# Kernel optimization log

Hardware: AMD Instinct MI355X
Metric: run time of the kernel (lower is better)

Reference implementation:

```python
import jax, jax.numpy as jnp
import numpy as np

N_NODES = 50000   # nodes per channel
N_EDGES = 800000  # intra edges per channel (avg degree ~16)
N_GRAPHS = 64     # graphs in the batch (global_add_pool segments)
D = 128           # node_features_len == out_channels
L = 3             # n_layers
BN_EPS = 1e-5
NEG_SLOPE = 0.01  # F.leaky_relu default


def setup_inputs() -> dict:
    key = jax.random.key(0)
    ks = jax.random.split(key, 24)
    s = 0.05
    inp = {
        "x1": jax.random.normal(ks[0], (N_NODES, D), jnp.float32),
        "x2": jax.random.normal(ks[1], (N_NODES, D), jnp.float32),
        # GIN MLP channel 1: Linear-BN-ReLU-Linear-ReLU, stacked over layers
        "W1_ch1": jax.random.normal(ks[2], (L, D, D), jnp.float32) * s,
        "b1_ch1": jax.random.normal(ks[3], (L, D), jnp.float32) * s,
        "bn_g": 1.0 + jax.random.normal(ks[4], (L, D), jnp.float32) * s,
        "bn_b": jax.random.normal(ks[5], (L, D), jnp.float32) * s,
        "bn_m": jax.random.normal(ks[6], (L, D), jnp.float32) * s,
        "bn_v": 0.5 + jax.random.uniform(ks[7], (L, D), jnp.float32),
        "W2_ch1": jax.random.normal(ks[8], (L, D, D), jnp.float32) * s,
        "b2_ch1": jax.random.normal(ks[9], (L, D), jnp.float32) * s,
        # GIN MLP channel 2: Linear-ReLU-Linear
        "W1_ch2": jax.random.normal(ks[10], (L, D, D), jnp.float32) * s,
        "b1_ch2": jax.random.normal(ks[11], (L, D), jnp.float32) * s,
        "W2_ch2": jax.random.normal(ks[12], (L, D, D), jnp.float32) * s,
        "b2_ch2": jax.random.normal(ks[13], (L, D), jnp.float32) * s,
        # head: Linear(2*D*L -> D) - ReLU - Dropout - Linear(D -> 1)
        "Wf1": jax.random.normal(ks[14], (2 * D * L, D), jnp.float32) * s,
        "bf1": jax.random.normal(ks[15], (D,), jnp.float32) * s,
        "Wf2": jax.random.normal(ks[16], (D, 1), jnp.float32) * s,
        "bf2": jax.random.normal(ks[17], (1,), jnp.float32) * s,
        "edge1": jax.random.randint(ks[18], (2, N_EDGES), 0, N_NODES, dtype=jnp.int32),
        "edge2": jax.random.randint(ks[19], (2, N_EDGES), 0, N_NODES, dtype=jnp.int32),
        "batch1": jnp.sort(jax.random.randint(ks[20], (N_NODES,), 0, N_GRAPHS, dtype=jnp.int32)),
        "batch2": jnp.sort(jax.random.randint(ks[21], (N_NODES,), 0, N_GRAPHS, dtype=jnp.int32)),
    }
    return inp


def _aggregate(x, edge):
    # GINConv sum aggregation: message x[src] scattered to dst; eps=0 default
    return jax.ops.segment_sum(x[edge[0]], edge[1], num_segments=N_NODES)


def _channel1(x, edge, batch, W1, b1, g, b, m, v, W2, b2):
    pooled = []
    for i in range(L):
        h = (x + _aggregate(x, edge)) @ W1[i] + b1[i]
        h = (h - m[i]) * (g[i] / jnp.sqrt(v[i] + BN_EPS)) + b[i]  # eval-mode BN
        h = jax.nn.relu(h)
        h = jax.nn.relu(h @ W2[i] + b2[i])
        x = jax.nn.leaky_relu(h, NEG_SLOPE)
        pooled.append(jax.ops.segment_sum(x, batch, num_segments=N_GRAPHS))
    return jnp.concatenate(pooled, axis=-1)  # [G, D*L]


def _channel2(x, edge, batch, W1, b1, W2, b2):
    pooled = []
    for i in range(L):
        h = jax.nn.relu((x + _aggregate(x, edge)) @ W1[i] + b1[i])
        h = h @ W2[i] + b2[i]
        x = jax.nn.leaky_relu(h, NEG_SLOPE)
        pooled.append(jax.ops.segment_sum(x, batch, num_segments=N_GRAPHS))
    return jnp.concatenate(pooled, axis=-1)  # [G, D*L]


def reference(x1, x2, W1_ch1, b1_ch1, bn_g, bn_b, bn_m, bn_v, W2_ch1, b2_ch1,
              W1_ch2, b1_ch2, W2_ch2, b2_ch2, Wf1, bf1, Wf2, bf2,
              edge1, edge2, batch1, batch2):
    p1 = _channel1(x1, edge1, batch1, W1_ch1, b1_ch1, bn_g, bn_b, bn_m, bn_v, W2_ch1, b2_ch1)
    p2 = _channel2(x2, edge2, batch2, W1_ch2, b1_ch2, W2_ch2, b2_ch2)
    z = jnp.concatenate([p1, p2], axis=-1)  # [G, 2*D*L]
    h = jax.nn.relu(z @ Wf1 + bf1)          # dropout is identity in eval mode
    return h @ Wf2 + bf2                    # [G, 1]
```

## Files before the change

### kernel.cpp

```cpp
#include <hip/hip_runtime.h>

#define NN 50000
#define NE 800000
#define NG 64
#define DD 128
#define NL 3
#define ZW (2 * DD * NL)
#define NB2 128
#define NPB 391
#define CAP2 8192
#define CHUNK 4096
#define P1B 196
#define GB2 1024

typedef __attribute__((ext_vector_type(8))) short short8;
typedef __attribute__((ext_vector_type(4))) float f32x4;

__device__ inline unsigned short f2bf(float f) {
  unsigned int u = __float_as_uint(f);
  unsigned int r = (u + 0x7fffu + ((u >> 16) & 1u)) >> 16;
  return (unsigned short)r;
}

__global__ __launch_bounds__(256) void cvt_bf16_kernel(const float* __restrict__ in,
                                                       unsigned short* __restrict__ out, int n8) {
  int i = blockIdx.x * 256 + threadIdx.x;
  if (i >= n8) return;
  const float4* in4 = reinterpret_cast<const float4*>(in);
  float4 a = in4[2 * i], b = in4[2 * i + 1];
  uint4 o;
  o.x = (unsigned int)f2bf(a.x) | ((unsigned int)f2bf(a.y) << 16);
  o.y = (unsigned int)f2bf(a.z) | ((unsigned int)f2bf(a.w) << 16);
  o.z = (unsigned int)f2bf(b.x) | ((unsigned int)f2bf(b.y) << 16);
  o.w = (unsigned int)f2bf(b.z) | ((unsigned int)f2bf(b.w) << 16);
  reinterpret_cast<uint4*>(out)[i] = o;
}

__global__ __launch_bounds__(256) void cvt_wt_kernel(const float* __restrict__ in,
                                                     unsigned short* __restrict__ out) {
  __shared__ float tile[32][33];
  int mat = blockIdx.z;
  int k0 = blockIdx.x * 32, c0 = blockIdx.y * 32;
  int tx = threadIdx.x & 31, ty = threadIdx.x >> 5;
  const float* ip = in + mat * 16384;
  unsigned short* op = out + mat * 16384;
#pragma unroll
  for (int rr = 0; rr < 32; rr += 8)
    tile[ty + rr][tx] = ip[(k0 + ty + rr) * 128 + (c0 + tx)];
  __syncthreads();
#pragma unroll
  for (int rr = 0; rr < 32; rr += 8)
    op[(c0 + ty + rr) * 128 + (k0 + tx)] = f2bf(tile[tx][ty + rr]);
}

__global__ __launch_bounds__(256) void bucket_kernel(const int* __restrict__ e1,
                                                     const int* __restrict__ e2,
                                                     int* __restrict__ bcur,
                                                     uint2* __restrict__ pairs) {
  int ch = blockIdx.x >= P1B;
  int blk = blockIdx.x - ch * P1B;
  const int* E = ch ? e2 : e1;
  int base = blk * CHUNK;
  __shared__ int lcnt[NB2], gbase[NB2];
  for (int i = threadIdx.x; i < NB2; i += 256) lcnt[i] = 0;
  __syncthreads();
  int srcv[16], dstv[16], lrank[16];
#pragma unroll
  for (int k = 0; k < 16; k++) {
    int e = base + k * 256 + threadIdx.x;
    if (e < NE) {
      srcv[k] = E[e];
      dstv[k] = E[NE + e];
      lrank[k] = atomicAdd(&lcnt[dstv[k] / NPB], 1);
    } else dstv[k] = -1;
  }
  __syncthreads();
  for (int i = threadIdx.x; i < NB2; i += 256)
    gbase[i] = atomicAdd(&bcur[ch * NB2 + i], lcnt[i]);
  __syncthreads();
#pragma unroll
  for (int k = 0; k < 16; k++)
    if (dstv[k] >= 0) {
      int g = dstv[k] / NPB;
      pairs[(size_t)(ch * NB2 + g) * CAP2 + gbase[g] + lrank[k]] =
          make_uint2((unsigned)srcv[k], (unsigned)dstv[k]);
    }
}

__global__ __launch_bounds__(256) void scan_bcur_kernel(const int* __restrict__ bcur,
                                                        int* __restrict__ colbase) {
  __shared__ int s[256];
  int tid = threadIdx.x;
  int v = bcur[tid];
  s[tid] = v;
  __syncthreads();
  int segstart = tid & ~127;
  for (int o = 1; o < 128; o <<= 1) {
    int t = (tid - o >= segstart) ? s[tid - o] : 0;
    __syncthreads();
    s[tid] += t;
    __syncthreads();
  }
  colbase[tid] = s[tid] - v;
}

__global__ __launch_bounds__(256) void csr_build_kernel(const uint2* __restrict__ pairs,
                                                        const int* __restrict__ bcur,
                                                        const int* __restrict__ colbase,
                                                        int* __restrict__ rowptr,
                                                        int* __restrict__ col) {
  int g = blockIdx.x;
  int ch = g >> 7, b = g & 127;
  int node0 = b * NPB;
  int nloc = min(NPB, NN - node0);
  int count = bcur[g];
  int base = colbase[g];
  const uint2* p = pairs + (size_t)g * CAP2;
  __shared__ int hist[512], pref[512], cur[512], stmp[256];
  for (int i = threadIdx.x; i < 512; i += 256) hist[i] = 0;
  __syncthreads();
  for (int e = threadIdx.x; e < count; e += 256)
    atomicAdd(&hist[(int)p[e].y - node0], 1);
  __syncthreads();
  int t = threadIdx.x;
  int a0 = hist[2 * t], a1 = hist[2 * t + 1];
  int sum = a0 + a1;
  stmp[t] = sum;
  __syncthreads();
  for (int o = 1; o < 256; o <<= 1) {
    int tv = (t >= o) ? stmp[t - o] : 0;
    __syncthreads();
    stmp[t] += tv;
    __syncthreads();
  }
  int ex = stmp[t] - sum;
  pref[2 * t] = ex;       pref[2 * t + 1] = ex + a0;
  cur[2 * t] = ex;        cur[2 * t + 1] = ex + a0;
  __syncthreads();
  for (int i = threadIdx.x; i < nloc; i += 256)
    rowptr[ch * (NN + 1) + node0 + i] = base + pref[i];
  if (threadIdx.x == 0 && b == NB2 - 1) rowptr[ch * (NN + 1) + NN] = base + count;
  for (int e = threadIdx.x; e < count; e += 256) {
    uint2 pr = p[e];
    int pos = atomicAdd(&cur[(int)pr.y - node0], 1);
    col[ch * NE + base + pos] = (int)pr.x;
  }
}

__global__ __launch_bounds__(256) void gstart_kernel(const int* __restrict__ batch1,
                                                     const int* __restrict__ batch2,
                                                     int* __restrict__ gstart) {
  int t = threadIdx.x;
  if (t >= 2 * (NG + 1)) return;
  int ch = t / (NG + 1), g = t % (NG + 1);
  const int* b = ch ? batch2 : batch1;
  int lo = 0, hi = NN;
  while (lo < hi) {
    int m = (lo + hi) >> 1;
    if (b[m] < g) lo = m + 1; else hi = m;
  }
  gstart[t] = lo;
}

__global__ __launch_bounds__(256) void agg_kernel(const unsigned short* __restrict__ X,
                                                  const int* __restrict__ rowptr,
                                                  const int* __restrict__ col,
                                                  unsigned short* __restrict__ Y) {
  int node = blockIdx.x * 16 + (threadIdx.x >> 4);
  int lane = threadIdx.x & 15;
  int ch = node >= NN;
  int nl = node - ch * NN;
  const int* rp = rowptr + ch * (NN + 1);
  const int* cl = col + ch * NE;
  const uint4* X4 = reinterpret_cast<const uint4*>(X);
  size_t chbase = (size_t)ch * NN * 16;
  float acc[8];
  {
    uint4 sv = X4[(size_t)node * 16 + lane];
    unsigned int w[4] = {sv.x, sv.y, sv.z, sv.w};
#pragma unroll
    for (int q = 0; q < 4; q++) {
      acc[2 * q]     = __uint_as_float(w[q] << 16);
      acc[2 * q + 1] = __uint_as_float(w[q] & 0xffff0000u);
    }
  }
  int s = rp[nl], e = rp[nl + 1];
  int j = s;
  for (; j + 8 <= e; j += 8) {
    uint4 v[8];
#pragma unroll
    for (int q = 0; q < 8; q++)
      v[q] = X4[chbase + (size_t)cl[j + q] * 16 + lane];
#pragma unroll
    for (int q = 0; q < 8; q++) {
      unsigned int w[4] = {v[q].x, v[q].y, v[q].z, v[q].w};
#pragma unroll
      for (int t = 0; t < 4; t++) {
        acc[2 * t]     += __uint_as_float(w[t] << 16);
        acc[2 * t + 1] += __uint_as_float(w[t] & 0xffff0000u);
      }
    }
  }
  for (; j < e; ++j) {
    uint4 v = X4[chbase + (size_t)cl[j] * 16 + lane];
    unsigned int w[4] = {v.x, v.y, v.z, v.w};
#pragma unroll
    for (int t = 0; t < 4; t++) {
      acc[2 * t]     += __uint_as_float(w[t] << 16);
      acc[2 * t + 1] += __uint_as_float(w[t] & 0xffff0000u);
    }
  }
  uint4 o;
  unsigned int* ow = reinterpret_cast<unsigned int*>(&o);
#pragma unroll
  for (int q = 0; q < 4; q++)
    ow[q] = (unsigned int)f2bf(acc[2 * q]) | ((unsigned int)f2bf(acc[2 * q + 1]) << 16);
  reinterpret_cast<uint4*>(Y)[(size_t)node * 16 + lane] = o;
}

__global__ __launch_bounds__(256) void gemm_fused_kernel(
    const unsigned short* __restrict__ Y, unsigned short* __restrict__ X,
    const unsigned short* __restrict__ WT,
    const float* __restrict__ b1c1, const float* __restrict__ b1c2,
    const float* __restrict__ b2c1, const float* __restrict__ b2c2,
    const float* __restrict__ bng, const float* __restrict__ bnb,
    const float* __restrict__ bnm, const float* __restrict__ bnv, int layer) {
  __shared__ unsigned short hlds[16][136];
  int ch = blockIdx.x >= GB2;
  int lane = threadIdx.x & 63, wv = threadIdx.x >> 6;
  int l15 = lane & 15, lk = lane >> 4;
  int c0 = wv * 32;
  const unsigned short* W1 = WT + (size_t)(ch * 6 + layer) * 16384;
  const unsigned short* W2 = WT + (size_t)(ch * 6 + 3 + layer) * 16384;
  short8 w1f[2][4], w2f[2][4];
#pragma unroll
  for (int ct = 0; ct < 2; ct++)
#pragma unroll
    for (int kk = 0; kk < 4; kk++) {
      size_t boff = (size_t)(c0 + ct * 16 + l15) * 128 + kk * 32 + lk * 8;
      w1f[ct][kk] = *reinterpret_cast<const short8*>(W1 + boff);
      w2f[ct][kk] = *reinterpret_cast<const short8*>(W2 + boff);
    }
  const float* b1 = (ch ? b1c2 : b1c1) + layer * DD;
  const float* b2 = (ch ? b2c2 : b2c1) + layer * DD;
  float sc1[2], sh1[2], sh2[2];
#pragma unroll
  for (int ct = 0; ct < 2; ct++) {
    int colg = c0 + ct * 16 + l15;
    if (!ch) {
      float s = bng[layer * DD + colg] * rsqrtf(bnv[layer * DD + colg] + 1e-5f);
      sc1[ct] = s;
      sh1[ct] = (b1[colg] - bnm[layer * DD + colg]) * s + bnb[layer * DD + colg];
    } else {
      sc1[ct] = 1.f;
      sh1[ct] = b1[colg];
    }
    sh2[ct] = b2[colg];
  }
  for (int t = (ch ? blockIdx.x - GB2 : blockIdx.x); t < 3125; t += GB2) {
    int r0l = t * 16;
    size_t r0g = (size_t)ch * NN + r0l;
    const unsigned short* yp = Y + (r0g + l15) * 128 + lk * 8;
    short8 a0 = *reinterpret_cast<const short8*>(yp);
    short8 a1 = *reinterpret_cast<const short8*>(yp + 32);
    short8 a2 = *reinterpret_cast<const short8*>(yp + 64);
    short8 a3 = *reinterpret_cast<const short8*>(yp + 96);
#pragma unroll
    for (int ct = 0; ct < 2; ct++) {
      f32x4 acc = {0.f, 0.f, 0.f, 0.f};
      acc = __builtin_amdgcn_mfma_f32_16x16x32_bf16(a0, w1f[ct][0], acc, 0, 0, 0);
      acc = __builtin_amdgcn_mfma_f32_16x16x32_bf16(a1, w1f[ct][1], acc, 0, 0, 0);
      acc = __builtin_amdgcn_mfma_f32_16x16x32_bf16(a2, w1f[ct][2], acc, 0, 0, 0);
      acc = __builtin_amdgcn_mfma_f32_16x16x32_bf16(a3, w1f[ct][3], acc, 0, 0, 0);
      int colg = c0 + ct * 16 + l15;
#pragma unroll
      for (int r = 0; r < 4; r++) {
        float tv = fmaxf(acc[r] * sc1[ct] + sh1[ct], 0.f);
        hlds[lk * 4 + r][colg] = f2bf(tv);
      }
    }
    __syncthreads();
    short8 h0 = *reinterpret_cast<const short8*>(&hlds[l15][lk * 8]);
    short8 h1 = *reinterpret_cast<const short8*>(&hlds[l15][32 + lk * 8]);
    short8 h2 = *reinterpret_cast<const short8*>(&hlds[l15][64 + lk * 8]);
    short8 h3 = *reinterpret_cast<const short8*>(&hlds[l15][96 + lk * 8]);
#pragma unroll
    for (int ct = 0; ct < 2; ct++) {
      f32x4 acc = {0.f, 0.f, 0.f, 0.f};
      acc = __builtin_amdgcn_mfma_f32_16x16x32_bf16(h0, w2f[ct][0], acc, 0, 0, 0);
      acc = __builtin_amdgcn_mfma_f32_16x16x32_bf16(h1, w2f[ct][1], acc, 0, 0, 0);
      acc = __builtin_amdgcn_mfma_f32_16x16x32_bf16(h2, w2f[ct][2], acc, 0, 0, 0);
      acc = __builtin_amdgcn_mfma_f32_16x16x32_bf16(h3, w2f[ct][3], acc, 0, 0, 0);
      int colg = c0 + ct * 16 + l15;
#pragma unroll
      for (int r = 0; r < 4; r++) {
        float tv = acc[r] + sh2[ct];
        if (!ch) tv = fmaxf(tv, 0.f);
        else     tv = tv > 0.f ? tv : 0.01f * tv;
        X[(r0g + lk * 4 + r) * 128 + colg] = f2bf(tv);
      }
    }
    __syncthreads();
  }
}

__global__ __launch_bounds__(256) void pool_kernel(const unsigned short* __restrict__ X,
                                                   const int* __restrict__ gstart,
                                                   float* __restrict__ z, int layer) {
  int ch = blockIdx.x >> 6, g = blockIdx.x & 63;
  int r0 = gstart[ch * (NG + 1) + g], r1 = gstart[ch * (NG + 1) + g + 1];
  int c8 = threadIdx.x & 15, part = threadIdx.x >> 4;
  const uint4* X4 = reinterpret_cast<const uint4*>(X);
  size_t base = (size_t)ch * NN * 16 + c8;
  float acc[8];
#pragma unroll
  for (int q = 0; q < 8; q++) acc[q] = 0.f;
  int r = r0 + part;
  for (; r + 48 < r1; r += 64) {
    uint4 v0 = X4[base + (size_t)r * 16];
    uint4 v1 = X4[base + (size_t)(r + 16) * 16];
    uint4 v2 = X4[base + (size_t)(r + 32) * 16];
    uint4 v3 = X4[base + (size_t)(r + 48) * 16];
    unsigned int w0[4] = {v0.x, v0.y, v0.z, v0.w};
    unsigned int w1[4] = {v1.x, v1.y, v1.z, v1.w};
    unsigned int w2[4] = {v2.x, v2.y, v2.z, v2.w};
    unsigned int w3[4] = {v3.x, v3.y, v3.z, v3.w};
#pragma unroll
    for (int q = 0; q < 4; q++) {
      acc[2 * q]     += __uint_as_float(w0[q] << 16) + __uint_as_float(w1[q] << 16) +
                        __uint_as_float(w2[q] << 16) + __uint_as_float(w3[q] << 16);
      acc[2 * q + 1] += __uint_as_float(w0[q] & 0xffff0000u) + __uint_as_float(w1[q] & 0xffff0000u) +
                        __uint_as_float(w2[q] & 0xffff0000u) + __uint_as_float(w3[q] & 0xffff0000u);
    }
  }
  for (; r < r1; r += 16) {
    uint4 v = X4[base + (size_t)r * 16];
    unsigned int w[4] = {v.x, v.y, v.z, v.w};
#pragma unroll
    for (int q = 0; q < 4; q++) {
      acc[2 * q]     += __uint_as_float(w[q] << 16);
      acc[2 * q + 1] += __uint_as_float(w[q] & 0xffff0000u);
    }
  }
  __shared__ float zacc[16][128];
#pragma unroll
  for (int q = 0; q < 8; q++) zacc[part][c8 * 8 + q] = acc[q];
  __syncthreads();
  for (int s = 8; s > 0; s >>= 1) {
    if (part < s) {
#pragma unroll
      for (int q = 0; q < 8; q++)
        zacc[part][c8 * 8 + q] += zacc[part + s][c8 * 8 + q];
    }
    __syncthreads();
  }
  if (part == 0) {
#pragma unroll
    for (int q = 0; q < 8; q++) {
      int colw = c8 * 8 + q;
      z[(size_t)g * ZW + ch * DD * NL + layer * DD + colw] = zacc[0][colw];
    }
  }
}

__global__ __launch_bounds__(128) void head_kernel(const float* __restrict__ z,
                                                   const float* __restrict__ Wf1,
                                                   const float* __restrict__ bf1,
                                                   const float* __restrict__ Wf2,
                                                   const float* __restrict__ bf2,
                                                   float* __restrict__ out) {
  int g = blockIdx.x, t = threadIdx.x;
  const float* zr = z + (size_t)g * ZW;
  float acc = bf1[t];
  for (int j = 0; j < ZW; ++j) acc += zr[j] * Wf1[(size_t)j * DD + t];
  float h = fmaxf(acc, 0.f);
  __shared__ float red[128];
  red[t] = h * Wf2[t];
  __syncthreads();
  for (int s = 64; s > 0; s >>= 1) {
    if (t < s) red[t] += red[t + s];
    __syncthreads();
  }
  if (t == 0) out[g] = red[0] + bf2[0];
}

extern "C" void kernel_launch(void* const* d_in, const int* in_sizes, int n_in,
                              void* d_out, int out_size, void* d_ws, size_t ws_size,
                              hipStream_t stream) {
  const float* x1   = (const float*)d_in[0];
  const float* x2   = (const float*)d_in[1];
  const float* W1c1 = (const float*)d_in[2];
  const float* b1c1 = (const float*)d_in[3];
  const float* bng  = (const float*)d_in[4];
  const float* bnb  = (const float*)d_in[5];
  const float* bnm  = (const float*)d_in[6];
  const float* bnv  = (const float*)d_in[7];
  const float* W2c1 = (const float*)d_in[8];
  const float* b2c1 = (const float*)d_in[9];
  const float* W1c2 = (const float*)d_in[10];
  const float* b1c2 = (const float*)d_in[11];
  const float* W2c2 = (const float*)d_in[12];
  const float* b2c2 = (const float*)d_in[13];
  const float* Wf1  = (const float*)d_in[14];
  const float* bf1  = (const float*)d_in[15];
  const float* Wf2  = (const float*)d_in[16];
  const float* bf2  = (const float*)d_in[17];
  const int* edge1  = (const int*)d_in[18];
  const int* edge2  = (const int*)d_in[19];
  const int* batch1 = (const int*)d_in[20];
  const int* batch2 = (const int*)d_in[21];
  (void)ws_size; (void)n_in; (void)in_sizes; (void)out_size;

  char* ws = (char*)d_ws;
  const size_t NB16 = (size_t)2 * NN * DD * 2;
  unsigned short* bufA = (unsigned short*)(ws);
  unsigned short* bufB = (unsigned short*)(ws + NB16);
  unsigned short* bufY = (unsigned short*)(ws + 2 * NB16);
  size_t off = 3 * NB16;
  unsigned short* WT = (unsigned short*)(ws + off); off += (size_t)12 * 16384 * 2;
  uint2* pairs = (uint2*)(ws + off); off += (size_t)2 * NB2 * CAP2 * 8;
  int* col     = (int*)(ws + off); off += (size_t)2 * NE * 4;
  int* rowptr  = (int*)(ws + off); off += (((size_t)2 * (NN + 1) * 4) + 255) & ~(size_t)255;
  int* bcur    = (int*)(ws + off); off += 256 * 4;
  int* colbase = (int*)(ws + off); off += 256 * 4;
  int* gstart  = (int*)(ws + off); off += 256 * 4;
  float* z     = (float*)(ws + off); off += (size_t)NG * ZW * 4;

  cvt_wt_kernel<<<dim3(4, 4, 3), 256, 0, stream>>>(W1c1, WT + 0 * 16384);
  cvt_wt_kernel<<<dim3(4, 4, 3), 256, 0, stream>>>(W2c1, WT + 3 * 16384);
  cvt_wt_kernel<<<dim3(4, 4, 3), 256, 0, stream>>>(W1c2, WT + 6 * 16384);
  cvt_wt_kernel<<<dim3(4, 4, 3), 256, 0, stream>>>(W2c2, WT + 9 * 16384);

  hipMemsetAsync(bcur, 0, 256 * 4, stream);

  cvt_bf16_kernel<<<(NN * DD / 8 + 255) / 256, 256, 0, stream>>>(x1, bufA, NN * DD / 8);
  cvt_bf16_kernel<<<(NN * DD / 8 + 255) / 256, 256, 0, stream>>>(x2, bufA + (size_t)NN * DD,
                                                                 NN * DD / 8);

  bucket_kernel<<<2 * P1B, 256, 0, stream>>>(edge1, edge2, bcur, pairs);
  scan_bcur_kernel<<<1, 256, 0, stream>>>(bcur, colbase);
  csr_build_kernel<<<2 * NB2, 256, 0, stream>>>(pairs, bcur, colbase, rowptr, col);
  gstart_kernel<<<1, 256, 0, stream>>>(batch1, batch2, gstart);

  unsigned short* cin = bufA;
  unsigned short* cout = bufB;
  for (int i = 0; i < NL; ++i) {
    agg_kernel<<<2 * NN / 16, 256, 0, stream>>>(cin, rowptr, col, bufY);
    gemm_fused_kernel<<<2 * GB2, 256, 0, stream>>>(bufY, cout, WT,
                                                   b1c1, b1c2, b2c1, b2c2,
                                                   bng, bnb, bnm, bnv, i);
    pool_kernel<<<2 * NG, 256, 0, stream>>>(cout, gstart, z, i);
    unsigned short* tmp = cin; cin = cout; cout = tmp;
  }

  head_kernel<<<NG, 128, 0, stream>>>(z, Wf1, bf1, Wf2, bf2, (float*)d_out);
}
```

Before: 388.9 us.

## Store node features in column-sliced layout so aggregation gathers hit smaller per-slice footprints

Node feature buffers are reorganized into 8 slices of 16 bf16 columns each, every slice laid out contiguously over all nodes. The aggregation kernel now handles one slice per block, so each gather reads 8 bytes per lane from a 3.2 MB slice region, aiming for better L2/MALL hit rates on the random neighbor reads. The GEMM, pooling and conversion kernels are updated to read and write the sliced layout. The trade-off is that CSR indices and rowptr are re-read once per slice, and each gather now moves 32-byte segments instead of full 256-byte rows.

```diff
diff --git a/kernel.cpp b/kernel.cpp
--- a/kernel.cpp
+++ b/kernel.cpp
@@ -2,6 +2,7 @@
 
 #define NN 50000
 #define NE 800000
+#define TOTN (2 * NN)
 #define NG 64
 #define DD 128
 #define NL 3
@@ -21,19 +22,26 @@
   unsigned int r = (u + 0x7fffu + ((u >> 16) & 1u)) >> 16;
   return (unsigned short)r;
 }
-
-__global__ __launch_bounds__(256) void cvt_bf16_kernel(const float* __restrict__ in,
-                                                       unsigned short* __restrict__ out, int n8) {
-  int i = blockIdx.x * 256 + threadIdx.x;
-  if (i >= n8) return;
-  const float4* in4 = reinterpret_cast<const float4*>(in);
-  float4 a = in4[2 * i], b = in4[2 * i + 1];
+__device__ inline float bflo(unsigned int u) { return __uint_as_float(u << 16); }
+__device__ inline float bfhi(unsigned int u) { return __uint_as_float(u & 0xffff0000u); }
+
+
+__global__ __launch_bounds__(256) void cvt_slice_kernel(const float* __restrict__ x1,
+                                                        const float* __restrict__ x2,
+                                                        unsigned short* __restrict__ Xs) {
+  int node = blockIdx.x * 16 + (threadIdx.x >> 4);
+  int c8 = threadIdx.x & 15;
+  int ch = node >= NN;
+  const float* x = ch ? x2 : x1;
+  int nl = node - ch * NN;
+  const float4* in4 = reinterpret_cast<const float4*>(x + (size_t)nl * 128 + c8 * 8);
+  float4 a = in4[0], b = in4[1];
   uint4 o;
   o.x = (unsigned int)f2bf(a.x) | ((unsigned int)f2bf(a.y) << 16);
   o.y = (unsigned int)f2bf(a.z) | ((unsigned int)f2bf(a.w) << 16);
   o.z = (unsigned int)f2bf(b.x) | ((unsigned int)f2bf(b.y) << 16);
   o.w = (unsigned int)f2bf(b.z) | ((unsigned int)f2bf(b.w) << 16);
-  reinterpret_cast<uint4*>(out)[i] = o;
+  *reinterpret_cast<uint4*>(Xs + ((size_t)(c8 >> 1) * TOTN + node) * 16 + (c8 & 1) * 8) = o;
 }
 
 __global__ __launch_bounds__(256) void cvt_wt_kernel(const float* __restrict__ in,
@@ -162,60 +170,47 @@
   gstart[t] = lo;
 }
 
-__global__ __launch_bounds__(256) void agg_kernel(const unsigned short* __restrict__ X,
-                                                  const int* __restrict__ rowptr,
-                                                  const int* __restrict__ col,
-                                                  unsigned short* __restrict__ Y) {
-  int node = blockIdx.x * 16 + (threadIdx.x >> 4);
-  int lane = threadIdx.x & 15;
+__global__ __launch_bounds__(256) void agg_slice_kernel(const unsigned short* __restrict__ Xs,
+                                                        const int* __restrict__ rowptr,
+                                                        const int* __restrict__ col,
+                                                        unsigned short* __restrict__ Ys) {
+  int slice = blockIdx.x & 7;
+  int node = (blockIdx.x >> 3) * 64 + (threadIdx.x >> 2);
+  if (node >= TOTN) return;
+  int lane4 = threadIdx.x & 3;
   int ch = node >= NN;
   int nl = node - ch * NN;
   const int* rp = rowptr + ch * (NN + 1);
   const int* cl = col + ch * NE;
-  const uint4* X4 = reinterpret_cast<const uint4*>(X);
-  size_t chbase = (size_t)ch * NN * 16;
-  float acc[8];
+  int srcoff = ch * NN;
+  const uint2* X2 = reinterpret_cast<const uint2*>(Xs + (size_t)slice * TOTN * 16);
+  float a0, a1, a2, a3;
   {
-    uint4 sv = X4[(size_t)node * 16 + lane];
-    unsigned int w[4] = {sv.x, sv.y, sv.z, sv.w};
-#pragma unroll
-    for (int q = 0; q < 4; q++) {
-      acc[2 * q]     = __uint_as_float(w[q] << 16);
-      acc[2 * q + 1] = __uint_as_float(w[q] & 0xffff0000u);
-    }
+    uint2 sv = X2[(size_t)node * 4 + lane4];
+    a0 = bflo(sv.x); a1 = bfhi(sv.x); a2 = bflo(sv.y); a3 = bfhi(sv.y);
   }
   int s = rp[nl], e = rp[nl + 1];
   int j = s;
   for (; j + 8 <= e; j += 8) {
-    uint4 v[8];
+    uint2 v[8];
 #pragma unroll
     for (int q = 0; q < 8; q++)
-      v[q] = X4[chbase + (size_t)cl[j + q] * 16 + lane];
+      v[q] = X2[(size_t)(srcoff + cl[j + q]) * 4 + lane4];
 #pragma unroll
     for (int q = 0; q < 8; q++) {
-      unsigned int w[4] = {v[q].x, v[q].y, v[q].z, v[q].w};
-#pragma unroll
-      for (int t = 0; t < 4; t++) {
-        acc[2 * t]     += __uint_as_float(w[t] << 16);
-        acc[2 * t + 1] += __uint_as_float(w[t] & 0xffff0000u);
-      }
+      a0 += bflo(v[q].x); a1 += bfhi(v[q].x);
+      a2 += bflo(v[q].y); a3 += bfhi(v[q].y);
     }
   }
   for (; j < e; ++j) {
-    uint4 v = X4[chbase + (size_t)cl[j] * 16 + lane];
-    unsigned int w[4] = {v.x, v.y, v.z, v.w};
-#pragma unroll
-    for (int t = 0; t < 4; t++) {
-      acc[2 * t]     += __uint_as_float(w[t] << 16);
-      acc[2 * t + 1] += __uint_as_float(w[t] & 0xffff0000u);
-    }
-  }
-  uint4 o;
-  unsigned int* ow = reinterpret_cast<unsigned int*>(&o);
-#pragma unroll
-  for (int q = 0; q < 4; q++)
-    ow[q] = (unsigned int)f2bf(acc[2 * q]) | ((unsigned int)f2bf(acc[2 * q + 1]) << 16);
-  reinterpret_cast<uint4*>(Y)[(size_t)node * 16 + lane] = o;
+    uint2 v = X2[(size_t)(srcoff + cl[j]) * 4 + lane4];
+    a0 += bflo(v.x); a1 += bfhi(v.x);
+    a2 += bflo(v.y); a3 += bfhi(v.y);
+  }
+  uint2 o;
+  o.x = (unsigned int)f2bf(a0) | ((unsigned int)f2bf(a1) << 16);
+  o.y = (unsigned int)f2bf(a2) | ((unsigned int)f2bf(a3) << 16);
+  reinterpret_cast<uint2*>(Ys + (size_t)slice * TOTN * 16)[(size_t)node * 4 + lane4] = o;
 }
 
 __global__ __launch_bounds__(256) void gemm_fused_kernel(
@@ -260,18 +255,18 @@
   for (int t = (ch ? blockIdx.x - GB2 : blockIdx.x); t < 3125; t += GB2) {
     int r0l = t * 16;
     size_t r0g = (size_t)ch * NN + r0l;
-    const unsigned short* yp = Y + (r0g + l15) * 128 + lk * 8;
-    short8 a0 = *reinterpret_cast<const short8*>(yp);
-    short8 a1 = *reinterpret_cast<const short8*>(yp + 32);
-    short8 a2 = *reinterpret_cast<const short8*>(yp + 64);
-    short8 a3 = *reinterpret_cast<const short8*>(yp + 96);
+    short8 a[4];
+#pragma unroll
+    for (int q = 0; q < 4; q++)
+      a[q] = *reinterpret_cast<const short8*>(
+          Y + ((size_t)(2 * q + (lk >> 1)) * TOTN + r0g + l15) * 16 + (lk & 1) * 8);
 #pragma unroll
     for (int ct = 0; ct < 2; ct++) {
       f32x4 acc = {0.f, 0.f, 0.f, 0.f};
-      acc = __builtin_amdgcn_mfma_f32_16x16x32_bf16(a0, w1f[ct][0], acc, 0, 0, 0);
-      acc = __builtin_amdgcn_mfma_f32_16x16x32_bf16(a1, w1f[ct][1], acc, 0, 0, 0);
-      acc = __builtin_amdgcn_mfma_f32_16x16x32_bf16(a2, w1f[ct][2], acc, 0, 0, 0);
-      acc = __builtin_amdgcn_mfma_f32_16x16x32_bf16(a3, w1f[ct][3], acc, 0, 0, 0);
+      acc = __builtin_amdgcn_mfma_f32_16x16x32_bf16(a[0], w1f[ct][0], acc, 0, 0, 0);
+      acc = __builtin_amdgcn_mfma_f32_16x16x32_bf16(a[1], w1f[ct][1], acc, 0, 0, 0);
+      acc = __builtin_amdgcn_mfma_f32_16x16x32_bf16(a[2], w1f[ct][2], acc, 0, 0, 0);
+      acc = __builtin_amdgcn_mfma_f32_16x16x32_bf16(a[3], w1f[ct][3], acc, 0, 0, 0);
       int colg = c0 + ct * 16 + l15;
 #pragma unroll
       for (int r = 0; r < 4; r++) {
@@ -292,12 +287,14 @@
       acc = __builtin_amdgcn_mfma_f32_16x16x32_bf16(h2, w2f[ct][2], acc, 0, 0, 0);
       acc = __builtin_amdgcn_mfma_f32_16x16x32_bf16(h3, w2f[ct][3], acc, 0, 0, 0);
       int colg = c0 + ct * 16 + l15;
+      size_t sb = (size_t)(colg >> 4) * TOTN;
+      int cw = colg & 15;
 #pragma unroll
       for (int r = 0; r < 4; r++) {
         float tv = acc[r] + sh2[ct];
         if (!ch) tv = fmaxf(tv, 0.f);
         else     tv = tv > 0.f ? tv : 0.01f * tv;
-        X[(r0g + lk * 4 + r) * 128 + colg] = f2bf(tv);
+        X[(sb + r0g + lk * 4 + r) * 16 + cw] = f2bf(tv);
       }
     }
     __syncthreads();
@@ -311,35 +308,33 @@
   int r0 = gstart[ch * (NG + 1) + g], r1 = gstart[ch * (NG + 1) + g + 1];
   int c8 = threadIdx.x & 15, part = threadIdx.x >> 4;
   const uint4* X4 = reinterpret_cast<const uint4*>(X);
-  size_t base = (size_t)ch * NN * 16 + c8;
+  size_t sb = ((size_t)(c8 >> 1) * TOTN + ch * NN) * 2 + (c8 & 1);
   float acc[8];
 #pragma unroll
   for (int q = 0; q < 8; q++) acc[q] = 0.f;
   int r = r0 + part;
   for (; r + 48 < r1; r += 64) {
-    uint4 v0 = X4[base + (size_t)r * 16];
-    uint4 v1 = X4[base + (size_t)(r + 16) * 16];
-    uint4 v2 = X4[base + (size_t)(r + 32) * 16];
-    uint4 v3 = X4[base + (size_t)(r + 48) * 16];
+    uint4 v0 = X4[sb + (size_t)r * 2];
+    uint4 v1 = X4[sb + (size_t)(r + 16) * 2];
+    uint4 v2 = X4[sb + (size_t)(r + 32) * 2];
+    uint4 v3 = X4[sb + (size_t)(r + 48) * 2];
     unsigned int w0[4] = {v0.x, v0.y, v0.z, v0.w};
     unsigned int w1[4] = {v1.x, v1.y, v1.z, v1.w};
     unsigned int w2[4] = {v2.x, v2.y, v2.z, v2.w};
     unsigned int w3[4] = {v3.x, v3.y, v3.z, v3.w};
 #pragma unroll
     for (int q = 0; q < 4; q++) {
-      acc[2 * q]     += __uint_as_float(w0[q] << 16) + __uint_as_float(w1[q] << 16) +
-                        __uint_as_float(w2[q] << 16) + __uint_as_float(w3[q] << 16);
-      acc[2 * q + 1] += __uint_as_float(w0[q] & 0xffff0000u) + __uint_as_float(w1[q] & 0xffff0000u) +
-                        __uint_as_float(w2[q] & 0xffff0000u) + __uint_as_float(w3[q] & 0xffff0000u);
+      acc[2 * q]     += bflo(w0[q]) + bflo(w1[q]) + bflo(w2[q]) + bflo(w3[q]);
+      acc[2 * q + 1] += bfhi(w0[q]) + bfhi(w1[q]) + bfhi(w2[q]) + bfhi(w3[q]);
     }
   }
   for (; r < r1; r += 16) {
-    uint4 v = X4[base + (size_t)r * 16];
+    uint4 v = X4[sb + (size_t)r * 2];
     unsigned int w[4] = {v.x, v.y, v.z, v.w};
 #pragma unroll
     for (int q = 0; q < 4; q++) {
-      acc[2 * q]     += __uint_as_float(w[q] << 16);
-      acc[2 * q + 1] += __uint_as_float(w[q] & 0xffff0000u);
+      acc[2 * q]     += bflo(w[q]);
+      acc[2 * q + 1] += bfhi(w[q]);
     }
   }
   __shared__ float zacc[16][128];
@@ -412,7 +407,7 @@
   (void)ws_size; (void)n_in; (void)in_sizes; (void)out_size;
 
   char* ws = (char*)d_ws;
-  const size_t NB16 = (size_t)2 * NN * DD * 2;
+  const size_t NB16 = (size_t)TOTN * DD * 2;
   unsigned short* bufA = (unsigned short*)(ws);
   unsigned short* bufB = (unsigned short*)(ws + NB16);
   unsigned short* bufY = (unsigned short*)(ws + 2 * NB16);
@@ -433,9 +428,7 @@
 
   hipMemsetAsync(bcur, 0, 256 * 4, stream);
 
-  cvt_bf16_kernel<<<(NN * DD / 8 + 255) / 256, 256, 0, stream>>>(x1, bufA, NN * DD / 8);
-  cvt_bf16_kernel<<<(NN * DD / 8 + 255) / 256, 256, 0, stream>>>(x2, bufA + (size_t)NN * DD,
-                                                                 NN * DD / 8);
+  cvt_slice_kernel<<<TOTN / 16, 256, 0, stream>>>(x1, x2, bufA);
 
   bucket_kernel<<<2 * P1B, 256, 0, stream>>>(edge1, edge2, bcur, pairs);
   scan_bcur_kernel<<<1, 256, 0, stream>>>(bcur, colbase);
@@ -444,8 +437,9 @@
 
   unsigned short* cin = bufA;
   unsigned short* cout = bufB;
+  const int AGG_GRID = ((TOTN + 63) / 64) * 8;
   for (int i = 0; i < NL; ++i) {
-    agg_kernel<<<2 * NN / 16, 256, 0, stream>>>(cin, rowptr, col, bufY);
+    agg_slice_kernel<<<AGG_GRID, 256, 0, stream>>>(cin, rowptr, col, bufY);
     gemm_fused_kernel<<<2 * GB2, 256, 0, stream>>>(bufY, cout, WT,
                                                    b1c1, b1c2, b2c1, b2c2,
                                                    bng, bnb, bnm, bnv, i);
```

New measurement: 411.8 us. +5.9%, slower.
